# Optimization experiments

Hardware: AMD Instinct MI355X
Metric: run time of the kernel (lower is better)

The kernel has to match this reference:

```python
import jax, jax.numpy as jnp
from jax import lax
import numpy as np

B, Hn, Wn = 128, 39, 39          # batch graphs, rows, cols (nodes per graph = Wn)
N = B * Wn                        # total nodes = 4992
HEADS, HID, OUT = 8, 64, 64
E_PER = 1563                      # edges per graph -> 200064 total
EPS = 1e-5                        # BatchNorm eps (eval mode, running mean=0 var=1)


def setup_inputs():
    key = jax.random.key(0)
    ks = jax.random.split(key, 32)
    rn = lambda k, shp, s: jax.random.normal(k, shp, jnp.float32) * s
    inp = {}
    inp['edge_index_batch'] = jax.random.randint(ks[0], (2, B, E_PER), 0, N)
    inp['ve_matrix_batch'] = rn(ks[1], (B, Hn, Wn), 1.0)
    inp['ac_matrix_batch'] = rn(ks[2], (B, Hn, Wn), 1.0)
    inp['man_matrix_batch'] = rn(ks[3], (B, Hn, Wn), 1.0)
    inp['mask_view_batch'] = jax.random.uniform(ks[4], (B, Wn, 1), jnp.float32)
    inp['graph_matrix'] = jnp.zeros((B, 2 * Hn, Wn), jnp.float32)
    # conv stack params
    inp['conv1_w'] = rn(ks[5], (8, 3, 1, 1), 1.0 / np.sqrt(3.0))
    inp['conv1_b'] = jnp.zeros((8,), jnp.float32)
    inp['bn1_g'] = jnp.ones((8,), jnp.float32)
    inp['bn1_b'] = jnp.zeros((8,), jnp.float32)
    inp['conv2_w'] = rn(ks[6], (16, 8, 3, 3), 1.0 / np.sqrt(8.0 * 9.0))
    inp['conv2_b'] = jnp.zeros((16,), jnp.float32)
    inp['bn2_g'] = jnp.ones((16,), jnp.float32)
    inp['bn2_b'] = jnp.zeros((16,), jnp.float32)
    # GRU(16 -> 1) params (torch layout: W_ih (3*h, in), W_hh (3*h, h))
    inp['gru_wih'] = rn(ks[7], (3, 16), 0.25)
    inp['gru_whh'] = rn(ks[8], (3, 1), 0.5)
    inp['gru_bih'] = jnp.zeros((3,), jnp.float32)
    inp['gru_bhh'] = jnp.zeros((3,), jnp.float32)
    # GATv2 layer 1: 78 -> (8 heads x 64)
    inp['g1_wl'] = rn(ks[9], (HEADS * HID, 78), 1.0 / np.sqrt(78.0))
    inp['g1_bl'] = jnp.zeros((HEADS * HID,), jnp.float32)
    inp['g1_wr'] = rn(ks[10], (HEADS * HID, 78), 1.0 / np.sqrt(78.0))
    inp['g1_br'] = jnp.zeros((HEADS * HID,), jnp.float32)
    inp['g1_att'] = rn(ks[11], (HEADS, HID), 1.0 / np.sqrt(HID))
    inp['g1_bias'] = jnp.zeros((HEADS * HID,), jnp.float32)
    # GATv2 layer 2: 512 -> (1 head x 64)
    inp['g2_wl'] = rn(ks[12], (OUT, HEADS * HID), 1.0 / np.sqrt(HEADS * HID))
    inp['g2_bl'] = jnp.zeros((OUT,), jnp.float32)
    inp['g2_wr'] = rn(ks[13], (OUT, HEADS * HID), 1.0 / np.sqrt(HEADS * HID))
    inp['g2_br'] = jnp.zeros((OUT,), jnp.float32)
    inp['g2_att'] = rn(ks[14], (1, OUT), 1.0 / np.sqrt(OUT))
    inp['g2_bias'] = jnp.zeros((OUT,), jnp.float32)
    return inp


def _conv2d(x, w, b, pad):
    y = lax.conv_general_dilated(x, w, (1, 1), [(pad, pad), (pad, pad)],
                                 dimension_numbers=('NCHW', 'OIHW', 'NCHW'))
    return y + b[None, :, None, None]


def _bn_eval(x, g, b):
    # eval-mode BatchNorm2d with fresh running stats (mean=0, var=1)
    return x * (g / jnp.sqrt(1.0 + EPS))[None, :, None, None] + b[None, :, None, None]


def _gatv2(x, src, dst, Wl, bl, Wr, br, att, bo, heads, ch):
    # PyG GATv2Conv: alpha = softmax_dst(att . leaky_relu(xl[src] + xr[dst]))
    xl = (x @ Wl.T + bl).reshape(-1, heads, ch)
    xr = (x @ Wr.T + br).reshape(-1, heads, ch)
    e = jax.nn.leaky_relu(xl[src] + xr[dst], 0.2)            # (E, heads, ch)
    logit = jnp.einsum('ehc,hc->eh', e, att)                 # (E, heads)
    m = jax.ops.segment_max(logit, dst, num_segments=N)
    ex = jnp.exp(logit - m[dst])
    den = jax.ops.segment_sum(ex, dst, num_segments=N)
    alpha = ex / den[dst]
    out = jax.ops.segment_sum(xl[src] * alpha[:, :, None], dst, num_segments=N)
    return out.reshape(-1, heads * ch) + bo


def reference(edge_index_batch, ve_matrix_batch, ac_matrix_batch, man_matrix_batch,
              mask_view_batch, graph_matrix, conv1_w, conv1_b, bn1_g, bn1_b,
              conv2_w, conv2_b, bn2_g, bn2_b, gru_wih, gru_whh, gru_bih, gru_bhh,
              g1_wl, g1_bl, g1_wr, g1_br, g1_att, g1_bias,
              g2_wl, g2_bl, g2_wr, g2_br, g2_att, g2_bias):
    man = jnp.where(jnp.isnan(man_matrix_batch), 0.0, man_matrix_batch)
    ac = jnp.where(jnp.isnan(ac_matrix_batch), 0.0, ac_matrix_batch)
    ve = jnp.where(jnp.isnan(ve_matrix_batch), 0.0, ve_matrix_batch)

    cm = jnp.stack([man, ac, ve], axis=1)                    # (B,3,H,W)
    x = jax.nn.relu(_bn_eval(_conv2d(cm, conv1_w, conv1_b, 0), bn1_g, bn1_b))
    x = _bn_eval(_conv2d(x, conv2_w, conv2_b, 1), bn2_g, bn2_b)  # (B,16,H,W); dropout=eval

    # GRU(16->1) over rows, batched across (graph, column) instead of a python loop
    xs = jnp.transpose(x, (2, 0, 3, 1)).reshape(Hn, B * Wn, 16)  # (T=H, B*W, 16)

    def step(h, xt):
        gi = xt @ gru_wih.T + gru_bih                        # (BW, 3)
        gh = h @ gru_whh.T + gru_bhh                         # (BW, 3)
        r = jax.nn.sigmoid(gi[:, 0:1] + gh[:, 0:1])
        z = jax.nn.sigmoid(gi[:, 1:2] + gh[:, 1:2])
        n = jnp.tanh(gi[:, 2:3] + r * gh[:, 2:3])
        hn = (1.0 - z) * n + z * h
        return hn, hn

    h0 = jnp.zeros((B * Wn, 1), x.dtype)
    _, outs = lax.scan(step, h0, xs)                         # (H, B*W, 1)
    conv_enc1 = jnp.transpose(outs.reshape(Hn, B, Wn), (1, 0, 2))  # (B,H,W)

    mask = mask_view_batch.reshape(B, -1)[:, None, :]        # (B,1,W)
    conv_enc2 = conv_enc1 * mask
    man2 = man * mask
    g = jnp.concatenate([man2, conv_enc2], axis=1)           # (B,78,W)  (graph_matrix input is overwritten)
    xn = jnp.transpose(g, (0, 2, 1)).reshape(N, 2 * Hn)      # (N,78)

    edges = edge_index_batch.reshape(2, -1)
    loop = jnp.arange(N)                                     # PyG add_self_loops=True
    src = jnp.concatenate([edges[0], loop])
    dst = jnp.concatenate([edges[1], loop])

    h1 = jax.nn.elu(_gatv2(xn, src, dst, g1_wl, g1_bl, g1_wr, g1_br, g1_att, g1_bias, HEADS, HID))
    h2 = _gatv2(h1, src, dst, g2_wl, g2_bl, g2_wr, g2_br, g2_att, g2_bias, 1, OUT)
    return h2.reshape(B, Wn, OUT)                            # (128, 39, 64)
```

## Files before the change

kernel.cpp:

```cpp
#include <hip/hip_runtime.h>
#include <hip/hip_bf16.h>
#include <math.h>

#define HN 39
#define WN 39
#define NBATCH 128
#define NPIX (HN * WN)
#define NNODE (NBATCH * WN)
#define E_RAW 200064
#define E_TOT (E_RAW + NNODE)
#define F1 512
#define F2 64
#define CROWS 6

static __device__ __forceinline__ float nan0(float x) { return (x == x) ? x : 0.f; }
static __device__ __forceinline__ float sigmoid_f(float x) { return 1.f / (1.f + __expf(-x)); }
static __device__ __forceinline__ float tanh_f(float x) {
    float e = __expf(2.f * x);
    return 1.f - 2.f / (e + 1.f);
}

#define BN_RSQ 0.99999500003749969f

__global__ __launch_bounds__(256) void conv_kernel(
    const float* __restrict__ ve, const float* __restrict__ ac, const float* __restrict__ man,
    const float* __restrict__ c1w, const float* __restrict__ c1b,
    const float* __restrict__ bn1g, const float* __restrict__ bn1b,
    const float* __restrict__ c2w, const float* __restrict__ c2b,
    const float* __restrict__ bn2g, const float* __restrict__ bn2b,
    const float* __restrict__ wih, const float* __restrict__ bih,
    float* __restrict__ gi_out)
{
    __shared__ float y1[8][(CROWS + 2) * WN + 8];
    const int b = blockIdx.x;
    const int r0 = blockIdx.y * CROWS;
    const int tid = threadIdx.x;

    for (int p = tid; p < (CROWS + 2) * WN; p += 256) {
        const int row = p / WN;
        const int hh = r0 - 1 + row;
        if (hh < 0 || hh >= HN) continue;
        const int w = p - row * WN;
        const int gidx = b * NPIX + hh * WN + w;
        const float m = nan0(man[gidx]);
        const float a = nan0(ac[gidx]);
        const float v = nan0(ve[gidx]);
#pragma unroll
        for (int c = 0; c < 8; ++c) {
            float val = c1w[c * 3 + 0] * m + c1w[c * 3 + 1] * a + c1w[c * 3 + 2] * v + c1b[c];
            val = val * (bn1g[c] * BN_RSQ) + bn1b[c];
            y1[c][p] = fmaxf(val, 0.f);
        }
    }
    __syncthreads();

    for (int p = tid; p < CROWS * WN; p += 256) {
        const int h = r0 + p / WN;
        if (h >= HN) continue;
        const int w = p - (p / WN) * WN;
        float acc[16];
#pragma unroll
        for (int o = 0; o < 16; ++o) acc[o] = 0.f;
        for (int c = 0; c < 8; ++c) {
#pragma unroll
            for (int dy = 0; dy < 3; ++dy) {
                const int hh = h + dy - 1;
                if (hh < 0 || hh >= HN) continue;
                const int lrow = hh - r0 + 1;
#pragma unroll
                for (int dx = 0; dx < 3; ++dx) {
                    const int ww = w + dx - 1;
                    if (ww < 0 || ww >= WN) continue;
                    const float yv = y1[c][lrow * WN + ww];
#pragma unroll
                    for (int o = 0; o < 16; ++o)
                        acc[o] = fmaf(c2w[((o * 8 + c) * 3 + dy) * 3 + dx], yv, acc[o]);
                }
            }
        }
        float gi0 = bih[0], gi1 = bih[1], gi2 = bih[2];
#pragma unroll
        for (int o = 0; o < 16; ++o) {
            const float x2 = (acc[o] + c2b[o]) * (bn2g[o] * BN_RSQ) + bn2b[o];
            gi0 = fmaf(wih[0 * 16 + o], x2, gi0);
            gi1 = fmaf(wih[1 * 16 + o], x2, gi1);
            gi2 = fmaf(wih[2 * 16 + o], x2, gi2);
        }
        const int idx = (b * NPIX + h * WN + w) * 3;
        gi_out[idx + 0] = gi0;
        gi_out[idx + 1] = gi1;
        gi_out[idx + 2] = gi2;
    }
}

__global__ __launch_bounds__(256) void gru_xn_kernel(
    const float* __restrict__ gi, const float* __restrict__ whh, const float* __restrict__ bhh,
    const float* __restrict__ man, const float* __restrict__ maskv,
    float* __restrict__ xn)
{
    const int idx = blockIdx.x * 256 + threadIdx.x;
    if (idx >= NNODE) return;
    const int b = idx / WN, w = idx - (idx / WN) * WN;
    const float mk = maskv[idx];
    float* __restrict__ xrow = xn + (size_t)idx * 78;

    for (int k = 0; k < HN; ++k)
        xrow[k] = nan0(man[b * NPIX + k * WN + w]) * mk;

    const float wh0 = whh[0], wh1 = whh[1], wh2 = whh[2];
    const float bh0 = bhh[0], bh1 = bhh[1], bh2 = bhh[2];
    float h = 0.f;
    for (int t = 0; t < HN; ++t) {
        const float* g = gi + ((size_t)b * NPIX + t * WN + w) * 3;
        const float g0 = g[0], g1 = g[1], g2 = g[2];
        const float r = sigmoid_f(g0 + h * wh0 + bh0);
        const float z = sigmoid_f(g1 + h * wh1 + bh1);
        const float n = tanh_f(g2 + r * (h * wh2 + bh2));
        h = (1.f - z) * n + z * h;
        xrow[HN + t] = h * mk;
    }
}

__global__ __launch_bounds__(256) void edge_hist(const int* __restrict__ ei, int* __restrict__ counts)
{
    const int e = blockIdx.x * 256 + threadIdx.x;
    if (e >= E_TOT) return;
    const int d = (e < E_RAW) ? ei[E_RAW + e] : (e - E_RAW);
    atomicAdd(&counts[d], 1);
}

__global__ __launch_bounds__(256) void scan_kernel(const int* __restrict__ counts,
                                                   int* __restrict__ offsets, int* __restrict__ cursor)
{
    __shared__ int sums[256];
    const int tid = threadIdx.x;
    const int start = tid * 20;
    const int end = min(start + 20, NNODE);
    int s = 0;
    for (int i = start; i < end; ++i) s += counts[i];
    sums[tid] = s;
    __syncthreads();
    for (int off = 1; off < 256; off <<= 1) {
        int v = (tid >= off) ? sums[tid - off] : 0;
        __syncthreads();
        sums[tid] += v;
        __syncthreads();
    }
    int run = (tid == 0) ? 0 : sums[tid - 1];
    for (int i = start; i < end; ++i) {
        offsets[i] = run;
        cursor[i] = run;
        run += counts[i];
    }
    if (tid == 255) offsets[NNODE] = run;
}

__global__ __launch_bounds__(256) void edge_scatter(const int* __restrict__ ei,
                                                    int* __restrict__ cursor,
                                                    int* __restrict__ srcs)
{
    const int e = blockIdx.x * 256 + threadIdx.x;
    if (e >= E_TOT) return;
    int s, d;
    if (e < E_RAW) { s = ei[e]; d = ei[E_RAW + e]; }
    else           { s = d = e - E_RAW; }
    const int pos = atomicAdd(&cursor[d], 1);
    srcs[pos] = s;
}

template <int K, int NZ>
__global__ __launch_bounds__(256, 4) void gemm_kernel(
    const float* __restrict__ X,
    const float* __restrict__ Wl, const float* __restrict__ bl,
    const float* __restrict__ Wr, const float* __restrict__ br,
    float* __restrict__ Yl, float* __restrict__ Yr, int J)
{
    const int nyb = J >> 6;
    const int sel = (blockIdx.y >= nyb) ? 1 : 0;
    const int j0 = (blockIdx.y - sel * nyb) * 64;
    const float* __restrict__ W = sel ? Wr : Wl;
    const float* __restrict__ bias = sel ? br : bl;
    float* __restrict__ Y;
    if (NZ == 1) Y = sel ? Yr : Yl;
    else         Y = Yl + ((size_t)blockIdx.z * 2 + sel) * ((size_t)NNODE * J);

    __shared__ __align__(16) float Xs[32][68];
    __shared__ __align__(16) float Ws[32][68];

    const int kchunk = K / NZ;
    const int kbeg = blockIdx.z * kchunk;
    const int kend = (blockIdx.z == NZ - 1) ? K : kbeg + kchunk;

    const int m0 = blockIdx.x * 64;
    const int tid = threadIdx.x;
    const int ti = tid / 16, tj = tid & 15;
    const int lrow = tid >> 2;
    const int ks = (tid & 3) * 8;

    float acc[4][4];
#pragma unroll
    for (int i = 0; i < 4; ++i)
#pragma unroll
        for (int j = 0; j < 4; ++j) acc[i][j] = 0.f;

    for (int k0 = kbeg; k0 < kend; k0 += 32) {
        const float* xp = X + (size_t)(m0 + lrow) * K + k0 + ks;
        const float* wp = W + (size_t)(j0 + lrow) * K + k0 + ks;
#pragma unroll
        for (int q = 0; q < 8; ++q) {
            const int k = k0 + ks + q;
            Xs[ks + q][lrow] = (k < K) ? xp[q] : 0.f;
            Ws[ks + q][lrow] = (k < K) ? wp[q] : 0.f;
        }
        __syncthreads();
#pragma unroll 8
        for (int kk = 0; kk < 32; ++kk) {
            const float4 xv = *(const float4*)&Xs[kk][ti * 4];
            const float4 wv = *(const float4*)&Ws[kk][tj * 4];
            acc[0][0] = fmaf(xv.x, wv.x, acc[0][0]);
            acc[0][1] = fmaf(xv.x, wv.y, acc[0][1]);
            acc[0][2] = fmaf(xv.x, wv.z, acc[0][2]);
            acc[0][3] = fmaf(xv.x, wv.w, acc[0][3]);
            acc[1][0] = fmaf(xv.y, wv.x, acc[1][0]);
            acc[1][1] = fmaf(xv.y, wv.y, acc[1][1]);
            acc[1][2] = fmaf(xv.y, wv.z, acc[1][2]);
            acc[1][3] = fmaf(xv.y, wv.w, acc[1][3]);
            acc[2][0] = fmaf(xv.z, wv.x, acc[2][0]);
            acc[2][1] = fmaf(xv.z, wv.y, acc[2][1]);
            acc[2][2] = fmaf(xv.z, wv.z, acc[2][2]);
            acc[2][3] = fmaf(xv.z, wv.w, acc[2][3]);
            acc[3][0] = fmaf(xv.w, wv.x, acc[3][0]);
            acc[3][1] = fmaf(xv.w, wv.y, acc[3][1]);
            acc[3][2] = fmaf(xv.w, wv.z, acc[3][2]);
            acc[3][3] = fmaf(xv.w, wv.w, acc[3][3]);
        }
        __syncthreads();
    }
#pragma unroll
    for (int i = 0; i < 4; ++i) {
        const int m = m0 + ti * 4 + i;
#pragma unroll
        for (int j = 0; j < 4; ++j) {
            const int jj = j0 + tj * 4 + j;
            if (NZ == 1) Y[(size_t)m * J + jj] = acc[i][j] + bias[jj];
            else         Y[(size_t)m * J + jj] = acc[i][j];
        }
    }
}

template <int NZ>
__global__ __launch_bounds__(256) void reduce_kernel(
    const float* __restrict__ P, const float* __restrict__ bl, const float* __restrict__ br,
    float* __restrict__ Yl, float* __restrict__ Yr)
{
    const int idx = blockIdx.x * 256 + threadIdx.x;
    const int per_side = NNODE * 64 / 4;
    if (idx >= 2 * per_side) return;
    const int side = idx >= per_side;
    const int r = idx - side * per_side;
    const int j4 = (r & 15);

    const float4* __restrict__ P4 = (const float4*)P;
    float4 acc = P4[(size_t)side * per_side + r];
#pragma unroll
    for (int z = 1; z < NZ; ++z) {
        const float4 v = P4[((size_t)z * 2 + side) * per_side + r];
        acc.x += v.x; acc.y += v.y; acc.z += v.z; acc.w += v.w;
    }
    const float4 bv = *(const float4*)((side ? br : bl) + j4 * 4);
    acc.x += bv.x; acc.y += bv.y; acc.z += bv.z; acc.w += bv.w;
    ((float4*)(side ? Yr : Yl))[r] = acc;
}

template <int FDIM>
static __device__ __forceinline__ void gat_nomax(
    const float* __restrict__ xl, const int* __restrict__ srcs,
    int base, int deg, int hoff, int lane, float4 xrv, float4 av,
    float4& accOut, float& lOut)
{
    const int e4 = lane >> 4;
    const int c4 = lane & 15;
    float l = 0.f;
    float4 acc = make_float4(0.f, 0.f, 0.f, 0.f);

    for (int c0 = 0; c0 < deg; c0 += 8) {
        const int eA = c0 + e4;
        const int eB = c0 + 4 + e4;
        const int sA = srcs[base + min(eA, deg - 1)];
        const int sB = srcs[base + min(eB, deg - 1)];
        const float4 xaA = *(const float4*)(xl + (size_t)sA * FDIM + hoff + c4 * 4);
        const float4 xaB = *(const float4*)(xl + (size_t)sB * FDIM + hoff + c4 * 4);

        float a0 = xaA.x + xrv.x; a0 = fmaxf(a0, 0.2f * a0);
        float a1 = xaA.y + xrv.y; a1 = fmaxf(a1, 0.2f * a1);
        float a2 = xaA.z + xrv.z; a2 = fmaxf(a2, 0.2f * a2);
        float a3 = xaA.w + xrv.w; a3 = fmaxf(a3, 0.2f * a3);
        float pA = av.x * a0 + av.y * a1 + av.z * a2 + av.w * a3;
        float b0 = xaB.x + xrv.x; b0 = fmaxf(b0, 0.2f * b0);
        float b1 = xaB.y + xrv.y; b1 = fmaxf(b1, 0.2f * b1);
        float b2 = xaB.z + xrv.z; b2 = fmaxf(b2, 0.2f * b2);
        float b3 = xaB.w + xrv.w; b3 = fmaxf(b3, 0.2f * b3);
        float pB = av.x * b0 + av.y * b1 + av.z * b2 + av.w * b3;

        pA += __shfl_xor(pA, 1, 64);
        pA += __shfl_xor(pA, 2, 64);
        pA += __shfl_xor(pA, 4, 64);
        pA += __shfl_xor(pA, 8, 64);
        pB += __shfl_xor(pB, 1, 64);
        pB += __shfl_xor(pB, 2, 64);
        pB += __shfl_xor(pB, 4, 64);
        pB += __shfl_xor(pB, 8, 64);

        const float wA = (eA < deg) ? __expf(pA) : 0.f;
        const float wB = (eB < deg) ? __expf(pB) : 0.f;
        l += wA + wB;
        acc.x = fmaf(wA, xaA.x, fmaf(wB, xaB.x, acc.x));
        acc.y = fmaf(wA, xaA.y, fmaf(wB, xaB.y, acc.y));
        acc.z = fmaf(wA, xaA.z, fmaf(wB, xaB.z, acc.z));
        acc.w = fmaf(wA, xaA.w, fmaf(wB, xaB.w, acc.w));
    }

    l += __shfl_xor(l, 16, 64);
    l += __shfl_xor(l, 32, 64);
    acc.x += __shfl_xor(acc.x, 16, 64);
    acc.y += __shfl_xor(acc.y, 16, 64);
    acc.z += __shfl_xor(acc.z, 16, 64);
    acc.w += __shfl_xor(acc.w, 16, 64);
    acc.x += __shfl_xor(acc.x, 32, 64);
    acc.y += __shfl_xor(acc.y, 32, 64);
    acc.z += __shfl_xor(acc.z, 32, 64);
    acc.w += __shfl_xor(acc.w, 32, 64);
    accOut = acc;
    lOut = l;
}

__global__ __launch_bounds__(512) void gat1_fused_kernel(
    const float* __restrict__ xl, const float* __restrict__ xr,
    const float* __restrict__ att, const float* __restrict__ bias,
    const int* __restrict__ offsets, const int* __restrict__ srcs,
    float* __restrict__ h1)
{
    const int n = blockIdx.x;
    const int h = threadIdx.x >> 6;
    const int lane = threadIdx.x & 63;
    const int base = offsets[n];
    const int deg = offsets[n + 1] - base;
    const int c4 = lane & 15;

    const float4 xrv = *(const float4*)(xr + (size_t)n * F1 + h * 64 + c4 * 4);
    const float4 av  = *(const float4*)(att + h * 64 + c4 * 4);

    float4 acc; float l;
    gat_nomax<F1>(xl, srcs, base, deg, h * 64, lane, xrv, av, acc, l);

    if ((lane >> 4) == 0) {
        const float inv = 1.f / l;
        const float4 bv = *(const float4*)(bias + h * 64 + c4 * 4);
        float4 o;
        o.x = acc.x * inv + bv.x; o.x = (o.x > 0.f) ? o.x : expm1f(o.x);
        o.y = acc.y * inv + bv.y; o.y = (o.y > 0.f) ? o.y : expm1f(o.y);
        o.z = acc.z * inv + bv.z; o.z = (o.z > 0.f) ? o.z : expm1f(o.z);
        o.w = acc.w * inv + bv.w; o.w = (o.w > 0.f) ? o.w : expm1f(o.w);
        *(float4*)(h1 + (size_t)n * F1 + h * 64 + c4 * 4) = o;
    }
}

__global__ __launch_bounds__(256) void gat2_fused_kernel(
    const float* __restrict__ xl, const float* __restrict__ xr,
    const float* __restrict__ att, const float* __restrict__ bias,
    const int* __restrict__ offsets, const int* __restrict__ srcs,
    float* __restrict__ out)
{
    const int wv = threadIdx.x >> 6;
    const int lane = threadIdx.x & 63;
    const int n = blockIdx.x * 4 + wv;
    const int base = offsets[n];
    const int deg = offsets[n + 1] - base;
    const int c4 = lane & 15;

    const float4 xrv = *(const float4*)(xr + (size_t)n * F2 + c4 * 4);
    const float4 av  = *(const float4*)(att + c4 * 4);

    float4 acc; float l;
    gat_nomax<F2>(xl, srcs, base, deg, 0, lane, xrv, av, acc, l);

    if ((lane >> 4) == 0) {
        const float inv = 1.f / l;
        const float4 bv = *(const float4*)(bias + c4 * 4);
        float4 o;
        o.x = acc.x * inv + bv.x;
        o.y = acc.y * inv + bv.y;
        o.z = acc.z * inv + bv.z;
        o.w = acc.w * inv + bv.w;
        *(float4*)(out + (size_t)n * F2 + c4 * 4) = o;
    }
}

extern "C" void kernel_launch(void* const* d_in, const int* in_sizes, int n_in,
                              void* d_out, int out_size, void* d_ws, size_t ws_size,
                              hipStream_t stream)
{
    const int*   ei    = (const int*)d_in[0];
    const float* ve    = (const float*)d_in[1];
    const float* ac    = (const float*)d_in[2];
    const float* man   = (const float*)d_in[3];
    const float* maskv = (const float*)d_in[4];
    const float* c1w   = (const float*)d_in[6];
    const float* c1b   = (const float*)d_in[7];
    const float* bn1g  = (const float*)d_in[8];
    const float* bn1b  = (const float*)d_in[9];
    const float* c2w   = (const float*)d_in[10];
    const float* c2b   = (const float*)d_in[11];
    const float* bn2g  = (const float*)d_in[12];
    const float* bn2b  = (const float*)d_in[13];
    const float* wih   = (const float*)d_in[14];
    const float* whh   = (const float*)d_in[15];
    const float* bih   = (const float*)d_in[16];
    const float* bhh   = (const float*)d_in[17];
    const float* g1wl  = (const float*)d_in[18];
    const float* g1bl  = (const float*)d_in[19];
    const float* g1wr  = (const float*)d_in[20];
    const float* g1br  = (const float*)d_in[21];
    const float* g1att = (const float*)d_in[22];
    const float* g1bias= (const float*)d_in[23];
    const float* g2wl  = (const float*)d_in[24];
    const float* g2bl  = (const float*)d_in[25];
    const float* g2wr  = (const float*)d_in[26];
    const float* g2br  = (const float*)d_in[27];
    const float* g2att = (const float*)d_in[28];
    const float* g2bias= (const float*)d_in[29];
    float* outp = (float*)d_out;

    float* ws     = (float*)d_ws;
    float* gi     = ws;
    float* xn     = gi     + 584064;
    float* xl1    = xn     + 389376;
    float* xr1    = xl1    + 2555904;
    float* h1     = xr1    + 2555904;
    float* xl2    = h1     + 2555904;
    float* xr2    = xl2    + 319488;
    int* counts  = (int*)(xr2 + 319488);
    int* offsets = counts + NNODE;
    int* cursor  = offsets + NNODE + 1;
    int* srcs    = cursor + NNODE;

    float* part = xr1;

    hipMemsetAsync(counts, 0, NNODE * sizeof(int), stream);

    conv_kernel<<<dim3(NBATCH, (HN + CROWS - 1) / CROWS), 256, 0, stream>>>(
        ve, ac, man, c1w, c1b, bn1g, bn1b, c2w, c2b, bn2g, bn2b, wih, bih, gi);
    gru_xn_kernel<<<(NNODE + 255) / 256, 256, 0, stream>>>(gi, whh, bhh, man, maskv, xn);

    edge_hist<<<(E_TOT + 255) / 256, 256, 0, stream>>>(ei, counts);
    scan_kernel<<<1, 256, 0, stream>>>(counts, offsets, cursor);
    edge_scatter<<<(E_TOT + 255) / 256, 256, 0, stream>>>(ei, cursor, srcs);

    gemm_kernel<78, 1><<<dim3(NNODE / 64, 2 * (F1 / 64)), 256, 0, stream>>>(
        xn, g1wl, g1bl, g1wr, g1br, xl1, xr1, F1);

    gat1_fused_kernel<<<NNODE, 512, 0, stream>>>(xl1, xr1, g1att, g1bias, offsets, srcs, h1);

    gemm_kernel<512, 4><<<dim3(NNODE / 64, 2 * (F2 / 64), 4), 256, 0, stream>>>(
        h1, g2wl, g2bl, g2wr, g2br, part, nullptr, F2);
    reduce_kernel<4><<<(2 * NNODE * 64 / 4 + 255) / 256, 256, 0, stream>>>(
        part, g2bl, g2br, xl2, xr2);

    gat2_fused_kernel<<<NNODE / 4, 256, 0, stream>>>(xl2, xr2, g2att, g2bias, offsets, srcs, outp);
}
```

Baseline: 315.6 us.

## Fuse man-to-xn copy into conv, restructure GRU gate layout, drop split-K reduce

The conv kernel now writes the masked man columns of xn directly, and stores the GRU input gates in planar (structure-of-arrays) layout so the GRU kernel reads them coalesced. The GRU kernel uses 64-thread blocks for more parallel blocks and is manually unrolled by three timesteps. The second-layer GEMM drops its split-K of 4 and the separate reduce kernel, saving a launch and a partial-sum round trip. The trade-off is less parallelism in that GEMM: only 156 blocks for a long K=512 loop.

After: 327.6 us. 3.8% more time.

```diff
diff --git a/kernel.cpp b/kernel.cpp
--- a/kernel.cpp
+++ b/kernel.cpp
@@ -12,6 +12,7 @@
 #define F1 512
 #define F2 64
 #define CROWS 6
+#define GIPL (NBATCH * NPIX)
 
 static __device__ __forceinline__ float nan0(float x) { return (x == x) ? x : 0.f; }
 static __device__ __forceinline__ float sigmoid_f(float x) { return 1.f / (1.f + __expf(-x)); }
@@ -29,7 +30,9 @@
     const float* __restrict__ c2w, const float* __restrict__ c2b,
     const float* __restrict__ bn2g, const float* __restrict__ bn2b,
     const float* __restrict__ wih, const float* __restrict__ bih,
-    float* __restrict__ gi_out)
+    const float* __restrict__ maskv,
+    float* __restrict__ gi_out,
+    float* __restrict__ xn)
 {
     __shared__ float y1[8][(CROWS + 2) * WN + 8];
     const int b = blockIdx.x;
@@ -45,6 +48,8 @@
         const float m = nan0(man[gidx]);
         const float a = nan0(ac[gidx]);
         const float v = nan0(ve[gidx]);
+        if (hh >= r0 && hh < r0 + CROWS)
+            xn[(size_t)(b * WN + w) * 78 + hh] = m * maskv[b * WN + w];
 #pragma unroll
         for (int c = 0; c < 8; ++c) {
             float val = c1w[c * 3 + 0] * m + c1w[c * 3 + 1] * a + c1w[c * 3 + 2] * v + c1b[c];
@@ -86,38 +91,53 @@
             gi1 = fmaf(wih[1 * 16 + o], x2, gi1);
             gi2 = fmaf(wih[2 * 16 + o], x2, gi2);
         }
-        const int idx = (b * NPIX + h * WN + w) * 3;
-        gi_out[idx + 0] = gi0;
-        gi_out[idx + 1] = gi1;
-        gi_out[idx + 2] = gi2;
-    }
-}
-
-__global__ __launch_bounds__(256) void gru_xn_kernel(
+        const int idx = b * NPIX + h * WN + w;
+        gi_out[idx] = gi0;
+        gi_out[GIPL + idx] = gi1;
+        gi_out[2 * GIPL + idx] = gi2;
+    }
+}
+
+__global__ __launch_bounds__(64) void gru_kernel(
     const float* __restrict__ gi, const float* __restrict__ whh, const float* __restrict__ bhh,
-    const float* __restrict__ man, const float* __restrict__ maskv,
-    float* __restrict__ xn)
-{
-    const int idx = blockIdx.x * 256 + threadIdx.x;
+    const float* __restrict__ maskv, float* __restrict__ xn)
+{
+    const int idx = blockIdx.x * 64 + threadIdx.x;
     if (idx >= NNODE) return;
     const int b = idx / WN, w = idx - (idx / WN) * WN;
     const float mk = maskv[idx];
-    float* __restrict__ xrow = xn + (size_t)idx * 78;
-
-    for (int k = 0; k < HN; ++k)
-        xrow[k] = nan0(man[b * NPIX + k * WN + w]) * mk;
+    float* __restrict__ xrow = xn + (size_t)idx * 78 + HN;
+
+    const float* __restrict__ g0 = gi + b * NPIX + w;
+    const float* __restrict__ g1 = g0 + GIPL;
+    const float* __restrict__ g2 = g0 + 2 * GIPL;
 
     const float wh0 = whh[0], wh1 = whh[1], wh2 = whh[2];
     const float bh0 = bhh[0], bh1 = bhh[1], bh2 = bhh[2];
     float h = 0.f;
-    for (int t = 0; t < HN; ++t) {
-        const float* g = gi + ((size_t)b * NPIX + t * WN + w) * 3;
-        const float g0 = g[0], g1 = g[1], g2 = g[2];
-        const float r = sigmoid_f(g0 + h * wh0 + bh0);
-        const float z = sigmoid_f(g1 + h * wh1 + bh1);
-        const float n = tanh_f(g2 + r * (h * wh2 + bh2));
+#pragma unroll 1
+    for (int t = 0; t < HN; t += 3) {
+        const float ga0 = g0[t * WN],       ga1 = g1[t * WN],       ga2 = g2[t * WN];
+        const float gb0 = g0[(t + 1) * WN], gb1 = g1[(t + 1) * WN], gb2 = g2[(t + 1) * WN];
+        const float gc0 = g0[(t + 2) * WN], gc1 = g1[(t + 2) * WN], gc2 = g2[(t + 2) * WN];
+
+        float r = sigmoid_f(ga0 + h * wh0 + bh0);
+        float z = sigmoid_f(ga1 + h * wh1 + bh1);
+        float n = tanh_f(ga2 + r * (h * wh2 + bh2));
         h = (1.f - z) * n + z * h;
-        xrow[HN + t] = h * mk;
+        xrow[t] = h * mk;
+
+        r = sigmoid_f(gb0 + h * wh0 + bh0);
+        z = sigmoid_f(gb1 + h * wh1 + bh1);
+        n = tanh_f(gb2 + r * (h * wh2 + bh2));
+        h = (1.f - z) * n + z * h;
+        xrow[t + 1] = h * mk;
+
+        r = sigmoid_f(gc0 + h * wh0 + bh0);
+        z = sigmoid_f(gc1 + h * wh1 + bh1);
+        n = tanh_f(gc2 + r * (h * wh2 + bh2));
+        h = (1.f - z) * n + z * h;
+        xrow[t + 2] = h * mk;
     }
 }
 
@@ -246,30 +266,6 @@
             else         Y[(size_t)m * J + jj] = acc[i][j];
         }
     }
-}
-
-template <int NZ>
-__global__ __launch_bounds__(256) void reduce_kernel(
-    const float* __restrict__ P, const float* __restrict__ bl, const float* __restrict__ br,
-    float* __restrict__ Yl, float* __restrict__ Yr)
-{
-    const int idx = blockIdx.x * 256 + threadIdx.x;
-    const int per_side = NNODE * 64 / 4;
-    if (idx >= 2 * per_side) return;
-    const int side = idx >= per_side;
-    const int r = idx - side * per_side;
-    const int j4 = (r & 15);
-
-    const float4* __restrict__ P4 = (const float4*)P;
-    float4 acc = P4[(size_t)side * per_side + r];
-#pragma unroll
-    for (int z = 1; z < NZ; ++z) {
-        const float4 v = P4[((size_t)z * 2 + side) * per_side + r];
-        acc.x += v.x; acc.y += v.y; acc.z += v.z; acc.w += v.w;
-    }
-    const float4 bv = *(const float4*)((side ? br : bl) + j4 * 4);
-    acc.x += bv.x; acc.y += bv.y; acc.z += bv.z; acc.w += bv.w;
-    ((float4*)(side ? Yr : Yl))[r] = acc;
 }
 
 template <int FDIM>
@@ -444,13 +440,12 @@
     int* cursor  = offsets + NNODE + 1;
     int* srcs    = cursor + NNODE;
 
-    float* part = xr1;
-
     hipMemsetAsync(counts, 0, NNODE * sizeof(int), stream);
 
     conv_kernel<<<dim3(NBATCH, (HN + CROWS - 1) / CROWS), 256, 0, stream>>>(
-        ve, ac, man, c1w, c1b, bn1g, bn1b, c2w, c2b, bn2g, bn2b, wih, bih, gi);
-    gru_xn_kernel<<<(NNODE + 255) / 256, 256, 0, stream>>>(gi, whh, bhh, man, maskv, xn);
+        ve, ac, man, c1w, c1b, bn1g, bn1b, c2w, c2b, bn2g, bn2b, wih, bih,
+        maskv, gi, xn);
+    gru_kernel<<<(NNODE + 63) / 64, 64, 0, stream>>>(gi, whh, bhh, maskv, xn);
 
     edge_hist<<<(E_TOT + 255) / 256, 256, 0, stream>>>(ei, counts);
     scan_kernel<<<1, 256, 0, stream>>>(counts, offsets, cursor);
@@ -461,10 +456,8 @@
 
     gat1_fused_kernel<<<NNODE, 512, 0, stream>>>(xl1, xr1, g1att, g1bias, offsets, srcs, h1);
 
-    gemm_kernel<512, 4><<<dim3(NNODE / 64, 2 * (F2 / 64), 4), 256, 0, stream>>>(
-        h1, g2wl, g2bl, g2wr, g2br, part, nullptr, F2);
-    reduce_kernel<4><<<(2 * NNODE * 64 / 4 + 255) / 256, 256, 0, stream>>>(
-        part, g2bl, g2br, xl2, xr2);
+    gemm_kernel<512, 1><<<dim3(NNODE / 64, 2 * (F2 / 64)), 256, 0, stream>>>(
+        h1, g2wl, g2bl, g2wr, g2br, xl2, xr2, F2);
 
     gat2_fused_kernel<<<NNODE / 4, 256, 0, stream>>>(xl2, xr2, g2att, g2bias, offsets, srcs, outp);
 }
```
